# Kernel tuning notes

Hardware: AMD Instinct MI355X
Metric: run time of the kernel (lower is better)

Reference implementation:

```python
import jax, jax.numpy as jnp
import numpy as np

N_NODES = 100000
N_EDGES = 1600000
N_GRAPHS = 64


def _sage(x, src, dst, Wl, bl, Wr):
    # SAGEConv (mean aggr): out = lin_l(mean_j x_j) + lin_r(x_i)
    msg = x[src]                                             # [E, F] gather
    s = jax.ops.segment_sum(msg, dst, num_segments=N_NODES)  # [N, F]
    cnt = jax.ops.segment_sum(jnp.ones((msg.shape[0],), x.dtype), dst,
                              num_segments=N_NODES)[:, None]
    mean = jnp.where(cnt > 0, s / jnp.maximum(cnt, 1.0), 0.0)
    return mean @ Wl + bl + x @ Wr


def setup_inputs() -> dict:
    key = jax.random.key(0)
    ks = jax.random.split(key, 12)
    sc = lambda f: 1.0 / np.sqrt(f)
    inp = {
        'x':   jax.random.normal(ks[0], (N_NODES, 32), jnp.float32),
        'Wl0': jax.random.normal(ks[1], (32, 64), jnp.float32) * sc(32),
        'bl0': jnp.zeros((64,), jnp.float32),
        'Wr0': jax.random.normal(ks[2], (32, 64), jnp.float32) * sc(32),
        'Wl1': jax.random.normal(ks[3], (64, 64), jnp.float32) * sc(64),
        'bl1': jnp.zeros((64,), jnp.float32),
        'Wr1': jax.random.normal(ks[4], (64, 64), jnp.float32) * sc(64),
        'Wl2': jax.random.normal(ks[5], (64, 64), jnp.float32) * sc(64),
        'bl2': jnp.zeros((64,), jnp.float32),
        'Wr2': jax.random.normal(ks[6], (64, 64), jnp.float32) * sc(64),
        'W_out': jax.random.normal(ks[7], (64, 8), jnp.float32) * sc(64),
        'b_out': jnp.zeros((8,), jnp.float32),
        'edge_index': jax.random.randint(ks[8], (2, N_EDGES), 0, N_NODES, jnp.int32),
        'batch': jnp.sort(jax.random.randint(ks[9], (N_NODES,), 0, N_GRAPHS, jnp.int32)),
    }
    return inp


def reference(x, Wl0, bl0, Wr0, Wl1, bl1, Wr1, Wl2, bl2, Wr2,
              W_out, b_out, edge_index, batch):
    src, dst = edge_index[0], edge_index[1]
    h = _sage(x, src, dst, Wl0, bl0, Wr0)
    h = _sage(h, src, dst, Wl1, bl1, Wr1)
    h = _sage(h, src, dst, Wl2, bl2, Wr2)
    pooled = jax.ops.segment_max(h, batch, num_segments=N_GRAPHS)  # [G, 64]
    logits = pooled @ W_out + b_out
    return jax.nn.log_softmax(logits, axis=-1)
```

## Files before the change

### kernel.cpp

```cpp
#include <hip/hip_runtime.h>
#include <math.h>
#include <stdint.h>

#define N_NODES 100000
#define N_EDGES 1600000
#define N_GRAPHS 64

#define BSH 9
#define NBKT 196
#define NCHUNK 256
#define EPC 6250
#define FLAT (NBKT * NCHUNK)


typedef __attribute__((ext_vector_type(8))) short bf16x8;
typedef __attribute__((ext_vector_type(8))) unsigned short u16x8;
typedef __attribute__((ext_vector_type(4))) float f32x4;

__device__ __forceinline__ void atomicMaxFloat(float* addr, float val) {
    if (val >= 0.0f) {
        atomicMax((int*)addr, __float_as_int(val));
    } else {
        atomicMin((unsigned int*)addr, __float_as_uint(val));
    }
}

__device__ __forceinline__ unsigned short f2bf(float f) {
    unsigned u = __float_as_uint(f);
    unsigned r = (u + 0x7FFFu + ((u >> 16) & 1u)) >> 16;
    return (unsigned short)r;
}
__device__ __forceinline__ float bf2f(unsigned short b) {
    return __uint_as_float(((unsigned)b) << 16);
}

__global__ __launch_bounds__(256) void k_prep(
    const float* __restrict__ x, unsigned short* __restrict__ xhi,
    const int* __restrict__ batch, int* __restrict__ gstart,
    float* __restrict__ pooled) {
    int i = blockIdx.x * blockDim.x + threadIdx.x;
    if (i < N_NODES * 32 / 8) {
        int base = i * 8;
        const float4* xp = (const float4*)(x + base);
        float4 a = xp[0], b = xp[1];
        u16x8 o;
        o[0] = f2bf(a.x); o[1] = f2bf(a.y); o[2] = f2bf(a.z); o[3] = f2bf(a.w);
        o[4] = f2bf(b.x); o[5] = f2bf(b.y); o[6] = f2bf(b.z); o[7] = f2bf(b.w);
        *(u16x8*)(xhi + base) = o;
    }
    if (i < N_GRAPHS * 64) pooled[i] = -INFINITY;
    if (i < N_NODES) {
        int b = batch[i];
        if (i == 0) {
            for (int g = 0; g <= b; ++g) gstart[g] = 0;
        } else {
            int pb = batch[i - 1];
            for (int g = pb + 1; g <= b; ++g) gstart[g] = i;
        }
        if (i == N_NODES - 1) {
            for (int g = b + 1; g <= N_GRAPHS; ++g) gstart[g] = N_NODES;
        }
    }
}

__global__ __launch_bounds__(256) void k_rhist(const int* __restrict__ dst,
                                               int* __restrict__ S) {
    __shared__ int h[NBKT];
    for (int i = threadIdx.x; i < NBKT; i += 256) h[i] = 0;
    __syncthreads();
    int c = blockIdx.x;
    int e0 = c * EPC;
    for (int e = e0 + threadIdx.x; e < e0 + EPC; e += 256)
        atomicAdd(&h[dst[e] >> BSH], 1);
    __syncthreads();
    for (int i = threadIdx.x; i < NBKT; i += 256) S[i * NCHUNK + c] = h[i];
}

__global__ __launch_bounds__(1024) void k_rscan(int* __restrict__ S) {
    __shared__ int part[1024];
    int t = threadIdx.x;
    const int seg = (FLAT + 1023) / 1024;
    int lo = t * seg;
    int hi = lo + seg; if (hi > FLAT) hi = FLAT;
    int s = 0;
    for (int i = lo; i < hi; ++i) s += S[i];
    part[t] = s;
    __syncthreads();
    for (int off = 1; off < 1024; off <<= 1) {
        int add = (t >= off) ? part[t - off] : 0;
        __syncthreads();
        part[t] += add;
        __syncthreads();
    }
    int ex = (t > 0) ? part[t - 1] : 0;
    if (t == 1023) S[FLAT] = part[1023];
    int run = ex;
    for (int i = lo; i < hi; ++i) { int v = S[i]; S[i] = run; run += v; }
}

__global__ __launch_bounds__(256) void k_rscatter(
    const int* __restrict__ src, const int* __restrict__ dst,
    const int* __restrict__ S, unsigned int* __restrict__ pairs) {
    __shared__ int ofs[NBKT];
    __shared__ int cnt[NBKT];
    int c = blockIdx.x;
    for (int i = threadIdx.x; i < NBKT; i += 256) {
        ofs[i] = S[i * NCHUNK + c];
        cnt[i] = 0;
    }
    __syncthreads();
    int e0 = c * EPC;
    for (int e = e0 + threadIdx.x; e < e0 + EPC; e += 256) {
        int d = dst[e];
        int b = d >> BSH;
        int r = atomicAdd(&cnt[b], 1);
        pairs[ofs[b] + r] = ((unsigned)(d & 511) << 17) | (unsigned)src[e];
    }
}

__global__ __launch_bounds__(256) void k_rbuild(
    const unsigned int* __restrict__ pairs, const int* __restrict__ S,
    int* __restrict__ row_ptr, int* __restrict__ col) {
    __shared__ int ncnt[512];
    __shared__ int nofs[512];
    __shared__ int part[256];
    int b = blockIdx.x;
    int t = threadIdx.x;
    int base = S[b * NCHUNK];
    int next = (b == NBKT - 1) ? S[FLAT] : S[(b + 1) * NCHUNK];
    int count = next - base;
    int nodeBase = b << BSH;

    ncnt[2 * t] = 0; ncnt[2 * t + 1] = 0;
    __syncthreads();
    for (int i = t; i < count; i += 256)
        atomicAdd(&ncnt[pairs[base + i] >> 17], 1);
    __syncthreads();
    int v0 = ncnt[2 * t], v1 = ncnt[2 * t + 1];
    part[t] = v0 + v1;
    __syncthreads();
    for (int off = 1; off < 256; off <<= 1) {
        int add = (t >= off) ? part[t - off] : 0;
        __syncthreads();
        part[t] += add;
        __syncthreads();
    }
    int ex = (t > 0) ? part[t - 1] : 0;
    nofs[2 * t] = ex;
    nofs[2 * t + 1] = ex + v0;
    ncnt[2 * t] = 0; ncnt[2 * t + 1] = 0;
    __syncthreads();
    for (int i = t; i < 512; i += 256) {
        int node = nodeBase + i;
        if (node < N_NODES) row_ptr[node] = base + nofs[i];
    }
    if (b == 0 && t == 0) row_ptr[N_NODES] = N_EDGES;
    for (int i = t; i < count; i += 256) {
        unsigned p = pairs[base + i];
        int li = p >> 17;
        int r = atomicAdd(&ncnt[li], 1);
        col[base + nofs[li] + r] = (int)(p & 0x1FFFFu);
    }
}

#define NC 8

template <int FIN>
__global__ __launch_bounds__(256) void k_agg_bf(
    const unsigned short* __restrict__ hb,
    const int* __restrict__ row_ptr, const int* __restrict__ col,
    float* __restrict__ mean) {
    int lane = threadIdx.x & 63;
    int wave = blockIdx.x * 4 + (threadIdx.x >> 6);
    int base = wave * NC;
    if (base >= N_NODES) return;
    int rp = row_ptr[base + (lane < NC ? lane : NC)];

    constexpr int G = (FIN == 64) ? 4 : 8;
    constexpr int LPR = 64 / G;
    int g  = lane / LPR;
    int fq = lane % LPR;

    for (int i = 0; i < NC; ++i) {
        int node = base + i;
        int start = __shfl(rp, i);
        int end   = __shfl(rp, i + 1);
        float s0 = 0.0f, s1 = 0.0f, s2 = 0.0f, s3 = 0.0f;

        for (int eb = start; eb < end; eb += 64) {
            int n = end - eb; if (n > 64) n = 64;
            int c = (eb + lane < end) ? col[eb + lane] : 0;
            int j = 0;
            for (; j + 4 * G - 1 < n; j += 4 * G) {
                int cA = __shfl(c, j + g);
                int cB = __shfl(c, j + G + g);
                int cC = __shfl(c, j + 2 * G + g);
                int cD = __shfl(c, j + 3 * G + g);
                ushort4 vA = *(const ushort4*)(hb + (size_t)cA * FIN + fq * 4);
                ushort4 vB = *(const ushort4*)(hb + (size_t)cB * FIN + fq * 4);
                ushort4 vC = *(const ushort4*)(hb + (size_t)cC * FIN + fq * 4);
                ushort4 vD = *(const ushort4*)(hb + (size_t)cD * FIN + fq * 4);
                s0 += (bf2f(vA.x) + bf2f(vB.x)) + (bf2f(vC.x) + bf2f(vD.x));
                s1 += (bf2f(vA.y) + bf2f(vB.y)) + (bf2f(vC.y) + bf2f(vD.y));
                s2 += (bf2f(vA.z) + bf2f(vB.z)) + (bf2f(vC.z) + bf2f(vD.z));
                s3 += (bf2f(vA.w) + bf2f(vB.w)) + (bf2f(vC.w) + bf2f(vD.w));
            }
            for (; j + 2 * G - 1 < n; j += 2 * G) {
                int cA = __shfl(c, j + g);
                int cB = __shfl(c, j + G + g);
                ushort4 vA = *(const ushort4*)(hb + (size_t)cA * FIN + fq * 4);
                ushort4 vB = *(const ushort4*)(hb + (size_t)cB * FIN + fq * 4);
                s0 += bf2f(vA.x) + bf2f(vB.x);
                s1 += bf2f(vA.y) + bf2f(vB.y);
                s2 += bf2f(vA.z) + bf2f(vB.z);
                s3 += bf2f(vA.w) + bf2f(vB.w);
            }
            for (; j + G - 1 < n; j += G) {
                int cA = __shfl(c, j + g);
                ushort4 vA = *(const ushort4*)(hb + (size_t)cA * FIN + fq * 4);
                s0 += bf2f(vA.x);
                s1 += bf2f(vA.y);
                s2 += bf2f(vA.z);
                s3 += bf2f(vA.w);
            }
            if (j < n) {
                int idx = j + g;
                bool valid = idx < n;
                int cA = __shfl(c, valid ? idx : 0);
                ushort4 vA = *(const ushort4*)(hb + (size_t)cA * FIN + fq * 4);
                if (valid) {
                    s0 += bf2f(vA.x);
                    s1 += bf2f(vA.y);
                    s2 += bf2f(vA.z);
                    s3 += bf2f(vA.w);
                }
            }
        }
#pragma unroll
        for (int m = LPR; m < 64; m <<= 1) {
            s0 += __shfl_xor(s0, m);
            s1 += __shfl_xor(s1, m);
            s2 += __shfl_xor(s2, m);
            s3 += __shfl_xor(s3, m);
        }
        int deg = end - start;
        float inv = (deg > 0) ? 1.0f / (float)deg : 0.0f;
        if (lane < LPR) {
            *(float4*)(mean + (size_t)node * 64 + fq * 4) =
                make_float4(s0 * inv, s1 * inv, s2 * inv, s3 * inv);
        }
    }
}

template <int KM, bool XBF, int KX, int XS, int OM>
__global__ __launch_bounds__(256) void k_dense_mfma(
    const float* mean,
    const float* x,
    const unsigned short* xhi, const unsigned short* xlo,
    const float* __restrict__ Wl, const float* __restrict__ bl,
    const float* __restrict__ Wr,
    float* outf, unsigned short* ohi, unsigned short* olo) {
    int lane = threadIdx.x & 63;
    int strip = blockIdx.x * 4 + (threadIdx.x >> 6);
    if (strip * 16 >= N_NODES) return;
    int row0 = strip * 16;
    int m = lane & 15;
    int g = lane >> 4;

    f32x4 acc[4] = {};

#pragma unroll
    for (int kt = 0; kt < KM / 32; ++kt) {
        int k0 = kt * 32 + g * 8;
        const float4* ap = (const float4*)(mean + (size_t)(row0 + m) * 64 + k0);
        float4 a0 = ap[0], a1 = ap[1];
        float av[8] = {a0.x, a0.y, a0.z, a0.w, a1.x, a1.y, a1.z, a1.w};
        bf16x8 ahi, alo;
#pragma unroll
        for (int j = 0; j < 8; ++j) {
            unsigned short hb = f2bf(av[j]);
            ahi[j] = (short)hb;
            alo[j] = (short)f2bf(av[j] - bf2f(hb));
        }
#pragma unroll
        for (int nt = 0; nt < 4; ++nt) {
            bf16x8 b;
#pragma unroll
            for (int j = 0; j < 8; ++j)
                b[j] = (short)f2bf(Wl[(size_t)(k0 + j) * 64 + nt * 16 + m]);
            acc[nt] = __builtin_amdgcn_mfma_f32_16x16x32_bf16(ahi, b, acc[nt], 0, 0, 0);
            acc[nt] = __builtin_amdgcn_mfma_f32_16x16x32_bf16(alo, b, acc[nt], 0, 0, 0);
        }
    }
#pragma unroll
    for (int kt = 0; kt < KX / 32; ++kt) {
        int k0 = kt * 32 + g * 8;
        bf16x8 ahi, alo;
        if constexpr (XBF) {
            ahi = *(const bf16x8*)(xhi + (size_t)(row0 + m) * XS + k0);
            alo = *(const bf16x8*)(xlo + (size_t)(row0 + m) * XS + k0);
        } else {
            const float4* ap = (const float4*)(x + (size_t)(row0 + m) * XS + k0);
            float4 a0 = ap[0], a1 = ap[1];
            float av[8] = {a0.x, a0.y, a0.z, a0.w, a1.x, a1.y, a1.z, a1.w};
#pragma unroll
            for (int j = 0; j < 8; ++j) {
                unsigned short hb = f2bf(av[j]);
                ahi[j] = (short)hb;
                alo[j] = (short)f2bf(av[j] - bf2f(hb));
            }
        }
#pragma unroll
        for (int nt = 0; nt < 4; ++nt) {
            bf16x8 b;
#pragma unroll
            for (int j = 0; j < 8; ++j)
                b[j] = (short)f2bf(Wr[(size_t)(k0 + j) * 64 + nt * 16 + m]);
            acc[nt] = __builtin_amdgcn_mfma_f32_16x16x32_bf16(ahi, b, acc[nt], 0, 0, 0);
            acc[nt] = __builtin_amdgcn_mfma_f32_16x16x32_bf16(alo, b, acc[nt], 0, 0, 0);
        }
    }
#pragma unroll
    for (int nt = 0; nt < 4; ++nt) {
        float bias = bl[nt * 16 + m];
#pragma unroll
        for (int r = 0; r < 4; ++r) {
            int row = row0 + g * 4 + r;
            float v = acc[nt][r] + bias;
            if constexpr (OM == 1) {
                unsigned short hb = f2bf(v);
                ohi[(size_t)row * 64 + nt * 16 + m] = hb;
                olo[(size_t)row * 64 + nt * 16 + m] = f2bf(v - bf2f(hb));
            } else if constexpr (OM == 2) {
                ohi[(size_t)row * 64 + nt * 16 + m] = f2bf(v);
            } else {
                outf[(size_t)row * 64 + nt * 16 + m] = v;
            }
        }
    }
}

#define PSPLIT 8
__global__ __launch_bounds__(256) void k_pool2(const unsigned short* __restrict__ h,
                                               const int* __restrict__ gstart,
                                               float* __restrict__ pooled) {
    __shared__ float red[4][64];
    int gr = blockIdx.x & 63;
    int split = blockIdx.x >> 6;
    int lane = threadIdx.x & 63;
    int w = threadIdx.x >> 6;
    int s = gstart[gr], e = gstart[gr + 1];
    float m = -INFINITY;
    for (int i = s + split * 4 + w; i < e; i += PSPLIT * 4)
        m = fmaxf(m, bf2f(h[(size_t)i * 64 + lane]));
    red[w][lane] = m;
    __syncthreads();
    if (w == 0) {
        m = fmaxf(fmaxf(red[0][lane], red[1][lane]),
                  fmaxf(red[2][lane], red[3][lane]));
        if (m > -INFINITY) atomicMaxFloat(&pooled[gr * 64 + lane], m);
    }
}

__global__ void k_head(const float* __restrict__ pooled,
                       const float* __restrict__ Wout,
                       const float* __restrict__ bout, float* __restrict__ out) {
    int tid = threadIdx.x;
    int g = tid >> 3, o = tid & 7;
    float acc = bout[o];
#pragma unroll
    for (int k = 0; k < 64; ++k) acc += pooled[g * 64 + k] * Wout[k * 8 + o];
    float mx = acc;
#pragma unroll
    for (int m = 1; m < 8; m <<= 1) mx = fmaxf(mx, __shfl_xor(mx, m));
    float ex = expf(acc - mx);
    float sum = ex;
#pragma unroll
    for (int m = 1; m < 8; m <<= 1) sum += __shfl_xor(sum, m);
    out[g * 8 + o] = (acc - mx) - logf(sum);
}

extern "C" void kernel_launch(void* const* d_in, const int* in_sizes, int n_in,
                              void* d_out, int out_size, void* d_ws, size_t ws_size,
                              hipStream_t stream) {
    const float* x    = (const float*)d_in[0];
    const float* Wl0  = (const float*)d_in[1];
    const float* bl0  = (const float*)d_in[2];
    const float* Wr0  = (const float*)d_in[3];
    const float* Wl1  = (const float*)d_in[4];
    const float* bl1  = (const float*)d_in[5];
    const float* Wr1  = (const float*)d_in[6];
    const float* Wl2  = (const float*)d_in[7];
    const float* bl2  = (const float*)d_in[8];
    const float* Wr2  = (const float*)d_in[9];
    const float* Wout = (const float*)d_in[10];
    const float* bout = (const float*)d_in[11];
    const int*   eidx = (const int*)d_in[12];
    const int*   batch= (const int*)d_in[13];
    const int* src = eidx;
    const int* dst = eidx + N_EDGES;

    uint8_t* ws = (uint8_t*)d_ws;
    int*   S       = (int*)(ws + 0);
    int*   row_ptr = (int*)(ws + 400128);
    int*   col     = (int*)(ws + 800256);
    float* pooled  = (float*)(ws + 7200384);
    int*   gstart  = (int*)(ws + 7216768);
    float* M       = (float*)(ws + 7217408);
    unsigned int* pairs = (unsigned int*)(ws + 7217408);
    unsigned short* Hhi = (unsigned short*)(ws + 32817408);
    unsigned short* Hlo = (unsigned short*)(ws + 45617408);

    k_prep<<<(N_NODES * 32 / 8 + 255) / 256, 256, 0, stream>>>(
        x, Hhi, batch, gstart, pooled);
    k_rhist<<<NCHUNK, 256, 0, stream>>>(dst, S);
    k_rscan<<<1, 1024, 0, stream>>>(S);
    k_rscatter<<<NCHUNK, 256, 0, stream>>>(src, dst, S, pairs);
    k_rbuild<<<NBKT, 256, 0, stream>>>(pairs, S, row_ptr, col);

    int aggBlocks = (N_NODES / NC + 3) / 4;
    int mfmaBlocks = (N_NODES / 16 + 3) / 4;

    k_agg_bf<32><<<aggBlocks, 256, 0, stream>>>(Hhi, row_ptr, col, M);
    k_dense_mfma<32, false, 32, 32, 1><<<mfmaBlocks, 256, 0, stream>>>(
        M, x, nullptr, nullptr, Wl0, bl0, Wr0, nullptr, Hhi, Hlo);
    k_agg_bf<64><<<aggBlocks, 256, 0, stream>>>(Hhi, row_ptr, col, M);
    k_dense_mfma<64, true, 64, 64, 1><<<mfmaBlocks, 256, 0, stream>>>(
        M, nullptr, Hhi, Hlo, Wl1, bl1, Wr1, nullptr, Hhi, Hlo);
    k_agg_bf<64><<<aggBlocks, 256, 0, stream>>>(Hhi, row_ptr, col, M);
    k_dense_mfma<64, true, 64, 64, 2><<<mfmaBlocks, 256, 0, stream>>>(
        M, nullptr, Hhi, Hlo, Wl2, bl2, Wr2, nullptr, Hhi, nullptr);

    k_pool2<<<64 * PSPLIT, 256, 0, stream>>>(Hhi, gstart, pooled);
    k_head<<<1, 512, 0, stream>>>(pooled, Wout, bout, (float*)d_out);
}
```

Measured before the change: 247.6 us.

## Fuse mean aggregation and dense MFMA into one SAGE kernel per layer

Merges the gather/mean kernel and the dense MFMA kernel into one kernel per layer. Each block handles two 16-row strips, builds the mean in shared memory, and splits the output columns across two waves after a barrier. This drops the fp32 mean round-trip through global memory and three kernel launches. In exchange, buffers are now double-buffered (ping-pong hi/lo) so later layers do not overwrite inputs still being gathered. Waves that finish aggregation early now wait at the barrier, and each wave's MFMA work is halved.

New measurement: 238.4 us. 3.7% less time.

```diff
diff --git a/kernel.cpp b/kernel.cpp
--- a/kernel.cpp
+++ b/kernel.cpp
@@ -163,133 +163,130 @@
     }
 }
 
-#define NC 8
-
-template <int FIN>
-__global__ __launch_bounds__(256) void k_agg_bf(
-    const unsigned short* __restrict__ hb,
+template <int KM, bool XBF, int KX, int XS, int OM>
+__global__ __launch_bounds__(256) void k_sage_fused(
+    const unsigned short* __restrict__ ghb,
+    const float* x,
+    const unsigned short* xhi, const unsigned short* xlo,
     const int* __restrict__ row_ptr, const int* __restrict__ col,
-    float* __restrict__ mean) {
+    const float* __restrict__ Wl, const float* __restrict__ bl,
+    const float* __restrict__ Wr,
+    unsigned short* ohi, unsigned short* olo) {
+    __shared__ float amean[2][KM][17];
+
     int lane = threadIdx.x & 63;
-    int wave = blockIdx.x * 4 + (threadIdx.x >> 6);
-    int base = wave * NC;
-    if (base >= N_NODES) return;
-    int rp = row_ptr[base + (lane < NC ? lane : NC)];
-
-    constexpr int G = (FIN == 64) ? 4 : 8;
-    constexpr int LPR = 64 / G;
-    int g  = lane / LPR;
-    int fq = lane % LPR;
-
-    for (int i = 0; i < NC; ++i) {
-        int node = base + i;
-        int start = __shfl(rp, i);
-        int end   = __shfl(rp, i + 1);
-        float s0 = 0.0f, s1 = 0.0f, s2 = 0.0f, s3 = 0.0f;
-
-        for (int eb = start; eb < end; eb += 64) {
-            int n = end - eb; if (n > 64) n = 64;
-            int c = (eb + lane < end) ? col[eb + lane] : 0;
-            int j = 0;
-            for (; j + 4 * G - 1 < n; j += 4 * G) {
-                int cA = __shfl(c, j + g);
-                int cB = __shfl(c, j + G + g);
-                int cC = __shfl(c, j + 2 * G + g);
-                int cD = __shfl(c, j + 3 * G + g);
-                ushort4 vA = *(const ushort4*)(hb + (size_t)cA * FIN + fq * 4);
-                ushort4 vB = *(const ushort4*)(hb + (size_t)cB * FIN + fq * 4);
-                ushort4 vC = *(const ushort4*)(hb + (size_t)cC * FIN + fq * 4);
-                ushort4 vD = *(const ushort4*)(hb + (size_t)cD * FIN + fq * 4);
-                s0 += (bf2f(vA.x) + bf2f(vB.x)) + (bf2f(vC.x) + bf2f(vD.x));
-                s1 += (bf2f(vA.y) + bf2f(vB.y)) + (bf2f(vC.y) + bf2f(vD.y));
-                s2 += (bf2f(vA.z) + bf2f(vB.z)) + (bf2f(vC.z) + bf2f(vD.z));
-                s3 += (bf2f(vA.w) + bf2f(vB.w)) + (bf2f(vC.w) + bf2f(vD.w));
-            }
-            for (; j + 2 * G - 1 < n; j += 2 * G) {
-                int cA = __shfl(c, j + g);
-                int cB = __shfl(c, j + G + g);
-                ushort4 vA = *(const ushort4*)(hb + (size_t)cA * FIN + fq * 4);
-                ushort4 vB = *(const ushort4*)(hb + (size_t)cB * FIN + fq * 4);
-                s0 += bf2f(vA.x) + bf2f(vB.x);
-                s1 += bf2f(vA.y) + bf2f(vB.y);
-                s2 += bf2f(vA.z) + bf2f(vB.z);
-                s3 += bf2f(vA.w) + bf2f(vB.w);
-            }
-            for (; j + G - 1 < n; j += G) {
-                int cA = __shfl(c, j + g);
-                ushort4 vA = *(const ushort4*)(hb + (size_t)cA * FIN + fq * 4);
-                s0 += bf2f(vA.x);
-                s1 += bf2f(vA.y);
-                s2 += bf2f(vA.z);
-                s3 += bf2f(vA.w);
-            }
-            if (j < n) {
-                int idx = j + g;
-                bool valid = idx < n;
-                int cA = __shfl(c, valid ? idx : 0);
-                ushort4 vA = *(const ushort4*)(hb + (size_t)cA * FIN + fq * 4);
-                if (valid) {
+    int wid  = threadIdx.x >> 6;
+    int sl   = wid >> 1;
+    int half = wid & 1;
+    int strip = blockIdx.x * 2 + sl;
+    int row0 = strip * 16;
+
+    {
+        constexpr int G = (KM == 64) ? 4 : 8;
+        constexpr int LPR = 64 / G;
+        int g  = lane / LPR;
+        int fq = lane % LPR;
+        int nodeBase = row0 + half * 8;
+        int rp = row_ptr[nodeBase + (lane < 8 ? lane : 8)];
+
+        for (int i = 0; i < 8; ++i) {
+            int start = __shfl(rp, i);
+            int end   = __shfl(rp, i + 1);
+            float s0 = 0.0f, s1 = 0.0f, s2 = 0.0f, s3 = 0.0f;
+
+            for (int eb = start; eb < end; eb += 64) {
+                int n = end - eb; if (n > 64) n = 64;
+                int c = (eb + lane < end) ? col[eb + lane] : 0;
+                int j = 0;
+                for (; j + 4 * G - 1 < n; j += 4 * G) {
+                    int cA = __shfl(c, j + g);
+                    int cB = __shfl(c, j + G + g);
+                    int cC = __shfl(c, j + 2 * G + g);
+                    int cD = __shfl(c, j + 3 * G + g);
+                    ushort4 vA = *(const ushort4*)(ghb + (size_t)cA * KM + fq * 4);
+                    ushort4 vB = *(const ushort4*)(ghb + (size_t)cB * KM + fq * 4);
+                    ushort4 vC = *(const ushort4*)(ghb + (size_t)cC * KM + fq * 4);
+                    ushort4 vD = *(const ushort4*)(ghb + (size_t)cD * KM + fq * 4);
+                    s0 += (bf2f(vA.x) + bf2f(vB.x)) + (bf2f(vC.x) + bf2f(vD.x));
+                    s1 += (bf2f(vA.y) + bf2f(vB.y)) + (bf2f(vC.y) + bf2f(vD.y));
+                    s2 += (bf2f(vA.z) + bf2f(vB.z)) + (bf2f(vC.z) + bf2f(vD.z));
+                    s3 += (bf2f(vA.w) + bf2f(vB.w)) + (bf2f(vC.w) + bf2f(vD.w));
+                }
+                for (; j + 2 * G - 1 < n; j += 2 * G) {
+                    int cA = __shfl(c, j + g);
+                    int cB = __shfl(c, j + G + g);
+                    ushort4 vA = *(const ushort4*)(ghb + (size_t)cA * KM + fq * 4);
+                    ushort4 vB = *(const ushort4*)(ghb + (size_t)cB * KM + fq * 4);
+                    s0 += bf2f(vA.x) + bf2f(vB.x);
+                    s1 += bf2f(vA.y) + bf2f(vB.y);
+                    s2 += bf2f(vA.z) + bf2f(vB.z);
+                    s3 += bf2f(vA.w) + bf2f(vB.w);
+                }
+                for (; j + G - 1 < n; j += G) {
+                    int cA = __shfl(c, j + g);
+                    ushort4 vA = *(const ushort4*)(ghb + (size_t)cA * KM + fq * 4);
                     s0 += bf2f(vA.x);
                     s1 += bf2f(vA.y);
                     s2 += bf2f(vA.z);
                     s3 += bf2f(vA.w);
                 }
+                if (j < n) {
+                    int idx = j + g;
+                    bool valid = idx < n;
+                    int cA = __shfl(c, valid ? idx : 0);
+                    ushort4 vA = *(const ushort4*)(ghb + (size_t)cA * KM + fq * 4);
+                    if (valid) {
+                        s0 += bf2f(vA.x);
+                        s1 += bf2f(vA.y);
+                        s2 += bf2f(vA.z);
+                        s3 += bf2f(vA.w);
+                    }
+                }
             }
-        }
-#pragma unroll
-        for (int m = LPR; m < 64; m <<= 1) {
-            s0 += __shfl_xor(s0, m);
-            s1 += __shfl_xor(s1, m);
-            s2 += __shfl_xor(s2, m);
-            s3 += __shfl_xor(s3, m);
-        }
-        int deg = end - start;
-        float inv = (deg > 0) ? 1.0f / (float)deg : 0.0f;
-        if (lane < LPR) {
-            *(float4*)(mean + (size_t)node * 64 + fq * 4) =
-                make_float4(s0 * inv, s1 * inv, s2 * inv, s3 * inv);
-        }
-    }
-}
-
-template <int KM, bool XBF, int KX, int XS, int OM>
-__global__ __launch_bounds__(256) void k_dense_mfma(
-    const float* mean,
-    const float* x,
-    const unsigned short* xhi, const unsigned short* xlo,
-    const float* __restrict__ Wl, const float* __restrict__ bl,
-    const float* __restrict__ Wr,
-    float* outf, unsigned short* ohi, unsigned short* olo) {
-    int lane = threadIdx.x & 63;
-    int strip = blockIdx.x * 4 + (threadIdx.x >> 6);
-    if (strip * 16 >= N_NODES) return;
-    int row0 = strip * 16;
+#pragma unroll
+            for (int m = LPR; m < 64; m <<= 1) {
+                s0 += __shfl_xor(s0, m);
+                s1 += __shfl_xor(s1, m);
+                s2 += __shfl_xor(s2, m);
+                s3 += __shfl_xor(s3, m);
+            }
+            int deg = end - start;
+            float inv = (deg > 0) ? 1.0f / (float)deg : 0.0f;
+            if (lane < LPR) {
+                int lr = half * 8 + i;
+                amean[sl][fq * 4 + 0][lr] = s0 * inv;
+                amean[sl][fq * 4 + 1][lr] = s1 * inv;
+                amean[sl][fq * 4 + 2][lr] = s2 * inv;
+                amean[sl][fq * 4 + 3][lr] = s3 * inv;
+            }
+        }
+    }
+    __syncthreads();
+
     int m = lane & 15;
     int g = lane >> 4;
-
-    f32x4 acc[4] = {};
+    f32x4 acc[2] = {};
 
 #pragma unroll
     for (int kt = 0; kt < KM / 32; ++kt) {
         int k0 = kt * 32 + g * 8;
-        const float4* ap = (const float4*)(mean + (size_t)(row0 + m) * 64 + k0);
-        float4 a0 = ap[0], a1 = ap[1];
-        float av[8] = {a0.x, a0.y, a0.z, a0.w, a1.x, a1.y, a1.z, a1.w};
         bf16x8 ahi, alo;
 #pragma unroll
         for (int j = 0; j < 8; ++j) {
-            unsigned short hb = f2bf(av[j]);
+            float v = amean[sl][k0 + j][m];
+            unsigned short hb = f2bf(v);
             ahi[j] = (short)hb;
-            alo[j] = (short)f2bf(av[j] - bf2f(hb));
-        }
-#pragma unroll
-        for (int nt = 0; nt < 4; ++nt) {
+            alo[j] = (short)f2bf(v - bf2f(hb));
+        }
+#pragma unroll
+        for (int nti = 0; nti < 2; ++nti) {
+            int nt = half * 2 + nti;
             bf16x8 b;
 #pragma unroll
             for (int j = 0; j < 8; ++j)
                 b[j] = (short)f2bf(Wl[(size_t)(k0 + j) * 64 + nt * 16 + m]);
-            acc[nt] = __builtin_amdgcn_mfma_f32_16x16x32_bf16(ahi, b, acc[nt], 0, 0, 0);
-            acc[nt] = __builtin_amdgcn_mfma_f32_16x16x32_bf16(alo, b, acc[nt], 0, 0, 0);
+            acc[nti] = __builtin_amdgcn_mfma_f32_16x16x32_bf16(ahi, b, acc[nti], 0, 0, 0);
+            acc[nti] = __builtin_amdgcn_mfma_f32_16x16x32_bf16(alo, b, acc[nti], 0, 0, 0);
         }
     }
 #pragma unroll
@@ -311,30 +308,30 @@
             }
         }
 #pragma unroll
-        for (int nt = 0; nt < 4; ++nt) {
+        for (int nti = 0; nti < 2; ++nti) {
+            int nt = half * 2 + nti;
             bf16x8 b;
 #pragma unroll
             for (int j = 0; j < 8; ++j)
                 b[j] = (short)f2bf(Wr[(size_t)(k0 + j) * 64 + nt * 16 + m]);
-            acc[nt] = __builtin_amdgcn_mfma_f32_16x16x32_bf16(ahi, b, acc[nt], 0, 0, 0);
-            acc[nt] = __builtin_amdgcn_mfma_f32_16x16x32_bf16(alo, b, acc[nt], 0, 0, 0);
-        }
-    }
-#pragma unroll
-    for (int nt = 0; nt < 4; ++nt) {
+            acc[nti] = __builtin_amdgcn_mfma_f32_16x16x32_bf16(ahi, b, acc[nti], 0, 0, 0);
+            acc[nti] = __builtin_amdgcn_mfma_f32_16x16x32_bf16(alo, b, acc[nti], 0, 0, 0);
+        }
+    }
+#pragma unroll
+    for (int nti = 0; nti < 2; ++nti) {
+        int nt = half * 2 + nti;
         float bias = bl[nt * 16 + m];
 #pragma unroll
         for (int r = 0; r < 4; ++r) {
             int row = row0 + g * 4 + r;
-            float v = acc[nt][r] + bias;
+            float v = acc[nti][r] + bias;
             if constexpr (OM == 1) {
                 unsigned short hb = f2bf(v);
                 ohi[(size_t)row * 64 + nt * 16 + m] = hb;
                 olo[(size_t)row * 64 + nt * 16 + m] = f2bf(v - bf2f(hb));
-            } else if constexpr (OM == 2) {
+            } else {
                 ohi[(size_t)row * 64 + nt * 16 + m] = f2bf(v);
-            } else {
-                outf[(size_t)row * 64 + nt * 16 + m] = v;
             }
         }
     }
@@ -406,31 +403,29 @@
     int*   col     = (int*)(ws + 800256);
     float* pooled  = (float*)(ws + 7200384);
     int*   gstart  = (int*)(ws + 7216768);
-    float* M       = (float*)(ws + 7217408);
-    unsigned int* pairs = (unsigned int*)(ws + 7217408);
-    unsigned short* Hhi = (unsigned short*)(ws + 32817408);
-    unsigned short* Hlo = (unsigned short*)(ws + 45617408);
+    unsigned short* H1hi = (unsigned short*)(ws + 7217408);
+    unsigned short* H1lo = (unsigned short*)(ws + 20017408);
+    unsigned short* H2hi = (unsigned short*)(ws + 32817408);
+    unsigned short* H2lo = (unsigned short*)(ws + 45617408);
+    unsigned int* pairs  = (unsigned int*)(ws + 32817408);
+    unsigned short* Xhi  = (unsigned short*)(ws + 45617408);
 
     k_prep<<<(N_NODES * 32 / 8 + 255) / 256, 256, 0, stream>>>(
-        x, Hhi, batch, gstart, pooled);
+        x, Xhi, batch, gstart, pooled);
     k_rhist<<<NCHUNK, 256, 0, stream>>>(dst, S);
     k_rscan<<<1, 1024, 0, stream>>>(S);
     k_rscatter<<<NCHUNK, 256, 0, stream>>>(src, dst, S, pairs);
     k_rbuild<<<NBKT, 256, 0, stream>>>(pairs, S, row_ptr, col);
 
-    int aggBlocks = (N_NODES / NC + 3) / 4;
-    int mfmaBlocks = (N_NODES / 16 + 3) / 4;
-
-    k_agg_bf<32><<<aggBlocks, 256, 0, stream>>>(Hhi, row_ptr, col, M);
-    k_dense_mfma<32, false, 32, 32, 1><<<mfmaBlocks, 256, 0, stream>>>(
-        M, x, nullptr, nullptr, Wl0, bl0, Wr0, nullptr, Hhi, Hlo);
-    k_agg_bf<64><<<aggBlocks, 256, 0, stream>>>(Hhi, row_ptr, col, M);
-    k_dense_mfma<64, true, 64, 64, 1><<<mfmaBlocks, 256, 0, stream>>>(
-        M, nullptr, Hhi, Hlo, Wl1, bl1, Wr1, nullptr, Hhi, Hlo);
-    k_agg_bf<64><<<aggBlocks, 256, 0, stream>>>(Hhi, row_ptr, col, M);
-    k_dense_mfma<64, true, 64, 64, 2><<<mfmaBlocks, 256, 0, stream>>>(
-        M, nullptr, Hhi, Hlo, Wl2, bl2, Wr2, nullptr, Hhi, nullptr);
-
-    k_pool2<<<64 * PSPLIT, 256, 0, stream>>>(Hhi, gstart, pooled);
+    int fusedBlocks = N_NODES / 32;
+
+    k_sage_fused<32, false, 32, 32, 1><<<fusedBlocks, 256, 0, stream>>>(
+        Xhi, x, nullptr, nullptr, row_ptr, col, Wl0, bl0, Wr0, H1hi, H1lo);
+    k_sage_fused<64, true, 64, 64, 1><<<fusedBlocks, 256, 0, stream>>>(
+        H1hi, nullptr, H1hi, H1lo, row_ptr, col, Wl1, bl1, Wr1, H2hi, H2lo);
+    k_sage_fused<64, true, 64, 64, 2><<<fusedBlocks, 256, 0, stream>>>(
+        H2hi, nullptr, H2hi, H2lo, row_ptr, col, Wl2, bl2, Wr2, H1hi, nullptr);
+
+    k_pool2<<<64 * PSPLIT, 256, 0, stream>>>(H1hi, gstart, pooled);
     k_head<<<1, 512, 0, stream>>>(pooled, Wout, bout, (float*)d_out);
 }
```
